# Performance work log

Measured on AMD Instinct MI355X. Metric: run time of the kernel, lower is better.

## Reference

```python
import jax, jax.numpy as jnp
import numpy as np

N0, N1, N2 = 120000, 40000, 10000   # sampled node counts per hop
E0, E1 = 600000, 150000             # edges per block (fanout ~15)
DIN, DH, NC = 128, 256, 47


def _glorot(k, fan_in, fan_out):
    s = (2.0 / (fan_in + fan_out)) ** 0.5
    return jax.random.normal(k, (fan_in, fan_out), jnp.float32) * s


def setup_inputs() -> dict:
    key = jax.random.key(0)
    ks = jax.random.split(key, 20)
    x0 = jax.random.normal(ks[0], (N0, DIN), jnp.float32)
    src0 = jax.random.randint(ks[1], (E0,), 0, N0)
    dst0 = jax.random.randint(ks[2], (E0,), 0, N1)
    src1 = jax.random.randint(ks[3], (E1,), 0, N1)
    dst1 = jax.random.randint(ks[4], (E1,), 0, N2)
    srcb0 = jax.random.randint(ks[5], (E0,), 0, N0)
    dstb0 = jax.random.randint(ks[6], (E0,), 0, N1)
    srcb1 = jax.random.randint(ks[7], (E1,), 0, N1)
    dstb1 = jax.random.randint(ks[8], (E1,), 0, N2)
    # id_old_value_new: must satisfy idx[:n] < n for every truncation length n,
    # i.e. idx[k] in [0, k+1)
    rng = np.random.default_rng(0)
    idx = jnp.asarray((rng.random(N0) * (np.arange(N0) + 1)).astype(np.int64))
    mix_ratio = jnp.float32(0.5)
    Wl0 = _glorot(ks[9], DIN, DH); Wr0 = _glorot(ks[10], DIN, DH)
    b0 = jnp.zeros((DH,), jnp.float32)
    Wl1 = _glorot(ks[11], DH, DH); Wr1 = _glorot(ks[12], DH, DH)
    b1 = jnp.zeros((DH,), jnp.float32)
    Wlin = _glorot(ks[13], DH, NC)
    blin = jnp.zeros((NC,), jnp.float32)
    return dict(x0=x0, src0=src0, dst0=dst0, src1=src1, dst1=dst1,
                srcb0=srcb0, dstb0=dstb0, srcb1=srcb1, dstb1=dstb1,
                idx=idx, mix_ratio=mix_ratio,
                Wl0=Wl0, Wr0=Wr0, b0=b0, Wl1=Wl1, Wr1=Wr1, b1=b1,
                Wlin=Wlin, blin=blin)


def _sage(x_all, root_x, src, dst, n_root, Wl, Wr, b):
    # PyG-style SAGEConv, mean aggregation: lin_l(mean_j x_j) + lin_r(root)
    msgs = x_all[src]                                        # [E, D] gather
    s = jax.ops.segment_sum(msgs, dst, num_segments=n_root)  # [n_root, D]
    cnt = jax.ops.segment_sum(jnp.ones_like(dst, dtype=x_all.dtype), dst,
                              num_segments=n_root)
    mean = s / jnp.maximum(cnt, 1.0)[:, None]
    return mean @ Wl + root_x @ Wr + b


def reference(x0, src0, dst0, src1, dst1, srcb0, dstb0, srcb1, dstb1,
              idx, mix_ratio, Wl0, Wr0, b0, Wl1, Wr1, b1, Wlin, blin):
    blocks = [(src0, dst0, N1), (src1, dst1, N2)]
    blocks_b = [(srcb0, dstb0, N1), (srcb1, dstb1, N2)]
    params = [(Wl0, Wr0, b0), (Wl1, Wr1, b1)]
    m = mix_ratio

    # first branch (dropout omitted: inference mode)
    aggr_xs = [x0]
    for i in range(2):
        src, dst, n_root = blocks[i]
        Wl, Wr, b = params[i]
        root_x = aggr_xs[-1][:n_root]
        x = jax.nn.relu(_sage(aggr_xs[-1], root_x, src, dst, n_root, Wl, Wr, b))
        aggr_xs.append(x)

    # permuted branch via id_old_value_new gather
    aggr_xs_b = [x[idx[: x.shape[0]]] for x in aggr_xs]

    x_mix = aggr_xs[0] * m + aggr_xs_b[0] * (1.0 - m)
    for i in range(2):
        src, dst, n_root = blocks[i]
        srcb, dstb, n_root_b = blocks_b[i]
        Wl, Wr, b = params[i]
        x_new = jax.nn.relu(_sage(aggr_xs[i], x_mix[:n_root], src, dst,
                                  n_root, Wl, Wr, b))
        x_new_b = jax.nn.relu(_sage(aggr_xs_b[i], x_mix[:n_root_b], srcb, dstb,
                                    n_root_b, Wl, Wr, b))
        x_mix = x_new * m + x_new_b * (1.0 - m)

    logits = x_mix @ Wlin + blin
    return jax.nn.log_softmax(logits, axis=-1)
```

## Files before the change

### kernel.cpp

```cpp
#include <hip/hip_runtime.h>
#include <math.h>

#define N1C 40000
#define N2C 10000
#define DIN 128
#define DH  256
#define NC  47

#define TOTCNT (2 * N1C + 2 * N2C)
#define CAP 64
#define CURSTR 16

typedef __attribute__((ext_vector_type(8))) short v8s;
typedef __attribute__((ext_vector_type(4))) float v4f;
typedef __attribute__((ext_vector_type(2))) float v2f;

#if __has_builtin(__builtin_amdgcn_cvt_pk_f32_fp8)
#define HW_FP8 1
#endif

__device__ __forceinline__ unsigned short f2bf(float f) {
    unsigned int u = __float_as_uint(f);
    u += 0x7FFF + ((u >> 16) & 1);
    return (unsigned short)(u >> 16);
}

__device__ __forceinline__ unsigned char f2e4m3(float f) {
    unsigned int u = __float_as_uint(f);
    unsigned char s = (unsigned char)((u >> 24) & 0x80);
    float a = __uint_as_float(u & 0x7FFFFFFF);
    if (a > 448.0f) a = 448.0f;
    if (a < 0.015625f) {
        int k = (int)rintf(a * 512.0f);
        return s | (unsigned char)k;
    }
    unsigned int bits = __float_as_uint(a);
    int et = (int)(bits >> 23) - 127 + 7;
    unsigned int m32 = bits & 0x7FFFFF;
    unsigned int m3 = m32 >> 20;
    unsigned int rest = m32 & 0xFFFFF;
    if (rest > 0x80000 || (rest == 0x80000 && (m3 & 1))) m3++;
    if (m3 == 8) { m3 = 0; et++; }
    if (et > 15 || (et == 15 && m3 == 7)) return s | 0x7E;
    return s | (unsigned char)((et << 3) | m3);
}

__device__ __forceinline__ unsigned int pack4_e4m3(float f0, float f1,
                                                   float f2, float f3) {
#if __has_builtin(__builtin_amdgcn_cvt_pk_fp8_f32)
    int q = __builtin_amdgcn_cvt_pk_fp8_f32(f0, f1, 0, false);
    q = __builtin_amdgcn_cvt_pk_fp8_f32(f2, f3, q, true);
    return (unsigned int)q;
#else
    return (unsigned int)f2e4m3(f0) | ((unsigned int)f2e4m3(f1) << 8) |
           ((unsigned int)f2e4m3(f2) << 16) | ((unsigned int)f2e4m3(f3) << 24);
#endif
}

__device__ __forceinline__ void dec4(unsigned int u, float& f0, float& f1,
                                     float& f2, float& f3) {
#ifdef HW_FP8
    v2f lo = __builtin_amdgcn_cvt_pk_f32_fp8((int)u, false);
    v2f hi = __builtin_amdgcn_cvt_pk_f32_fp8((int)u, true);
    f0 = lo[0]; f1 = lo[1]; f2 = hi[0]; f3 = hi[1];
#else
    auto d1 = [](unsigned int b) -> float {
        int e = (b >> 3) & 15, mm = b & 7;
        float d = (e == 0) ? (float)mm * (1.0f / 512.0f)
                           : (1.0f + (float)mm * 0.125f) * exp2f((float)(e - 7));
        return (b & 0x80) ? -d : d;
    };
    f0 = d1(u & 0xFF); f1 = d1((u >> 8) & 0xFF);
    f2 = d1((u >> 16) & 0xFF); f3 = d1(u >> 24);
#endif
}

__device__ __forceinline__ void acc16(uint4 q, float* a) {
    float f0, f1, f2, f3;
    dec4(q.x, f0, f1, f2, f3); a[0] += f0; a[1] += f1; a[2] += f2; a[3] += f3;
    dec4(q.y, f0, f1, f2, f3); a[4] += f0; a[5] += f1; a[6] += f2; a[7] += f3;
    dec4(q.z, f0, f1, f2, f3); a[8] += f0; a[9] += f1; a[10] += f2; a[11] += f3;
    dec4(q.w, f0, f1, f2, f3); a[12] += f0; a[13] += f1; a[14] += f2; a[15] += f3;
}

__global__ __launch_bounds__(256) void front_fused(
        const int* __restrict__ src0, const int* __restrict__ dst0,
        const int* __restrict__ srcb0, const int* __restrict__ dstb0,
        const int* __restrict__ src1, const int* __restrict__ dst1,
        const int* __restrict__ srcb1, const int* __restrict__ dstb1,
        const int* __restrict__ perm, int* __restrict__ cur,
        int* __restrict__ bucket, int E0, int E1, int nbMain,
        const float* __restrict__ x0, unsigned char* __restrict__ x0f,
        int n8,
        const float* __restrict__ Wl0, const float* __restrict__ Wr0,
        const float* __restrict__ Wl1, const float* __restrict__ Wr1,
        unsigned short* __restrict__ Wt0l, unsigned short* __restrict__ Wt0r,
        unsigned short* __restrict__ Wt1l, unsigned short* __restrict__ Wt1r) {
    int b = blockIdx.x, t = threadIdx.x;
    if (b < nbMain) {
        int gid = b * 256 + t;
        int tot = 2 * E0 + 2 * E1;
        bool doEdge = gid < tot;
        int s = 0, bin = 0, pos = CAP;
        if (doEdge) {
            if (gid < E0) {
                s = src0[gid];                bin = dst0[gid];
            } else if (gid < 2 * E0) {
                int le = gid - E0;
                s = perm[srcb0[le]];          bin = N1C + dstb0[le];
            } else if (gid < 2 * E0 + E1) {
                int le = gid - 2 * E0;
                s = src1[le];                 bin = 2 * N1C + dst1[le];
            } else {
                int le = gid - 2 * E0 - E1;
                s = perm[srcb1[le]];          bin = 2 * N1C + N2C + dstb1[le];
            }
            pos = atomicAdd(&cur[(size_t)bin * CURSTR], 1);
        }
        if (gid < n8) {
            const float4* p = (const float4*)(x0 + (size_t)gid * 8);
            float4 a = p[0], c = p[1];
            uint2 q;
            q.x = pack4_e4m3(a.x, a.y, a.z, a.w);
            q.y = pack4_e4m3(c.x, c.y, c.z, c.w);
            *(uint2*)(x0f + (size_t)gid * 8) = q;
        }
        if (doEdge && pos < CAP) bucket[(size_t)bin * CAP + pos] = s;
    } else {
        int id = (b - nbMain) * 256 + t;
        const int S0 = DIN * DH;
        const int S1 = DH * DH;
        const float* W; unsigned short* Wt; int K, loc;
        if (id < S0)                   { W = Wl0; Wt = Wt0l; K = DIN; loc = id; }
        else if (id < 2 * S0)          { W = Wr0; Wt = Wt0r; K = DIN; loc = id - S0; }
        else if (id < 2 * S0 + S1)     { W = Wl1; Wt = Wt1l; K = DH;  loc = id - 2 * S0; }
        else if (id < 2 * S0 + 2 * S1) { W = Wr1; Wt = Wt1r; K = DH;  loc = id - 2 * S0 - S1; }
        else return;
        int n = loc / K, k = loc - n * K;
        Wt[(size_t)n * K + k] = f2bf(W[(size_t)k * DH + n]);
    }
}

__global__ __launch_bounds__(256) void gather_mean_128f(
        const unsigned char* __restrict__ xf, const int* __restrict__ bucket,
        const int* __restrict__ cur, unsigned short* __restrict__ mean0,
        unsigned short* __restrict__ meanb0) {
    const int half = N1C / 32;
    int b = blockIdx.x;
    int binbase; unsigned short* outp; int rb;
    if (b < half) { binbase = 0;   outp = mean0;  rb = b; }
    else          { binbase = N1C; outp = meanb0; rb = b - half; }
    int wv = threadIdx.x >> 6, lane = threadIdx.x & 63;
    int row = rb * 32 + wv * 8 + (lane >> 3);
    int c16 = (lane & 7) * 16;
    int bin = binbase + row;
    int cnt = min(cur[(size_t)bin * CURSTR], CAP);
    const int* cs = bucket + (size_t)bin * CAP;
    float a[16];
#pragma unroll
    for (int j = 0; j < 16; j++) a[j] = 0.0f;
    int i = 0;
    for (; i + 3 < cnt; i += 4) {
        int s0 = cs[i], s1 = cs[i + 1], s2 = cs[i + 2], s3 = cs[i + 3];
        uint4 q0 = *(const uint4*)&xf[(size_t)s0 * DIN + c16];
        uint4 q1 = *(const uint4*)&xf[(size_t)s1 * DIN + c16];
        uint4 q2 = *(const uint4*)&xf[(size_t)s2 * DIN + c16];
        uint4 q3 = *(const uint4*)&xf[(size_t)s3 * DIN + c16];
        acc16(q0, a); acc16(q1, a); acc16(q2, a); acc16(q3, a);
    }
    for (; i < cnt; i++) {
        uint4 q = *(const uint4*)&xf[(size_t)cs[i] * DIN + c16];
        acc16(q, a);
    }
    float inv = 1.0f / (float)max(cnt, 1);
    uint4 o0, o1;
    o0.x = (unsigned int)f2bf(a[0] * inv)  | ((unsigned int)f2bf(a[1] * inv) << 16);
    o0.y = (unsigned int)f2bf(a[2] * inv)  | ((unsigned int)f2bf(a[3] * inv) << 16);
    o0.z = (unsigned int)f2bf(a[4] * inv)  | ((unsigned int)f2bf(a[5] * inv) << 16);
    o0.w = (unsigned int)f2bf(a[6] * inv)  | ((unsigned int)f2bf(a[7] * inv) << 16);
    o1.x = (unsigned int)f2bf(a[8] * inv)  | ((unsigned int)f2bf(a[9] * inv) << 16);
    o1.y = (unsigned int)f2bf(a[10] * inv) | ((unsigned int)f2bf(a[11] * inv) << 16);
    o1.z = (unsigned int)f2bf(a[12] * inv) | ((unsigned int)f2bf(a[13] * inv) << 16);
    o1.w = (unsigned int)f2bf(a[14] * inv) | ((unsigned int)f2bf(a[15] * inv) << 16);
    unsigned short* op = &outp[(size_t)row * DIN + c16];
    *(uint4*)op = o0;
    *(uint4*)(op + 8) = o1;
}

__global__ __launch_bounds__(256) void gather_mean_256f(
        const unsigned char* __restrict__ xf, const int* __restrict__ bucket,
        const int* __restrict__ cur, unsigned short* __restrict__ mean1,
        unsigned short* __restrict__ meanb1) {
    const int half = N2C / 16;
    int b = blockIdx.x;
    int binbase; unsigned short* outp; int rb;
    if (b < half) { binbase = 2 * N1C;       outp = mean1;  rb = b; }
    else          { binbase = 2 * N1C + N2C; outp = meanb1; rb = b - half; }
    int wv = threadIdx.x >> 6, lane = threadIdx.x & 63;
    int row = rb * 16 + wv * 4 + (lane >> 4);
    int c16 = (lane & 15) * 16;
    int bin = binbase + row;
    int cnt = min(cur[(size_t)bin * CURSTR], CAP);
    const int* cs = bucket + (size_t)bin * CAP;
    float a[16];
#pragma unroll
    for (int j = 0; j < 16; j++) a[j] = 0.0f;
    int i = 0;
    for (; i + 3 < cnt; i += 4) {
        int s0 = cs[i], s1 = cs[i + 1], s2 = cs[i + 2], s3 = cs[i + 3];
        uint4 q0 = *(const uint4*)&xf[(size_t)s0 * DH + c16];
        uint4 q1 = *(const uint4*)&xf[(size_t)s1 * DH + c16];
        uint4 q2 = *(const uint4*)&xf[(size_t)s2 * DH + c16];
        uint4 q3 = *(const uint4*)&xf[(size_t)s3 * DH + c16];
        acc16(q0, a); acc16(q1, a); acc16(q2, a); acc16(q3, a);
    }
    for (; i < cnt; i++) {
        uint4 q = *(const uint4*)&xf[(size_t)cs[i] * DH + c16];
        acc16(q, a);
    }
    float inv = 1.0f / (float)max(cnt, 1);
    uint4 o0, o1;
    o0.x = (unsigned int)f2bf(a[0] * inv)  | ((unsigned int)f2bf(a[1] * inv) << 16);
    o0.y = (unsigned int)f2bf(a[2] * inv)  | ((unsigned int)f2bf(a[3] * inv) << 16);
    o0.z = (unsigned int)f2bf(a[4] * inv)  | ((unsigned int)f2bf(a[5] * inv) << 16);
    o0.w = (unsigned int)f2bf(a[6] * inv)  | ((unsigned int)f2bf(a[7] * inv) << 16);
    o1.x = (unsigned int)f2bf(a[8] * inv)  | ((unsigned int)f2bf(a[9] * inv) << 16);
    o1.y = (unsigned int)f2bf(a[10] * inv) | ((unsigned int)f2bf(a[11] * inv) << 16);
    o1.z = (unsigned int)f2bf(a[12] * inv) | ((unsigned int)f2bf(a[13] * inv) << 16);
    o1.w = (unsigned int)f2bf(a[14] * inv) | ((unsigned int)f2bf(a[15] * inv) << 16);
    unsigned short* op = &outp[(size_t)row * DH + c16];
    *(uint4*)op = o0;
    *(uint4*)(op + 8) = o1;
}

#define KP0 136
#define H0T 5
__global__ __launch_bounds__(256, 2) void hop0_mfma(
        const float* __restrict__ x0, const int* __restrict__ idx,
        const unsigned short* __restrict__ mean0, const unsigned short* __restrict__ meanb0,
        const unsigned short* __restrict__ Wtl, const unsigned short* __restrict__ Wtr,
        const float* __restrict__ b, const float* __restrict__ mixp,
        unsigned char* __restrict__ x1f, unsigned short* __restrict__ xm1) {
    __shared__ unsigned short Alds[4][16][KP0];
    int t = threadIdx.x;
    int wv = t >> 6, lane = t & 63;
    int mrow = lane & 15, quad = lane >> 4;
    float m = *mixp;

    v8s wl[4][4], wr[4][4];
    float bb[4];
#pragma unroll
    for (int ct = 0; ct < 4; ct++) {
        int n = wv * 64 + mrow * 4 + ct;
        bb[ct] = b[n];
#pragma unroll
        for (int ks = 0; ks < 4; ks++) {
            int k0 = ks * 32 + quad * 8;
            wl[ct][ks] = *(const v8s*)&Wtl[(size_t)n * DIN + k0];
            wr[ct][ks] = *(const v8s*)&Wtr[(size_t)n * DIN + k0];
        }
    }

    for (int tile = 0; tile < H0T; tile++) {
        int row0 = (blockIdx.x * H0T + tile) * 16;
        {
            int r = t >> 4, k0 = (t & 15) * 8;
            int rg = row0 + r;
            *(v8s*)&Alds[0][r][k0] = *(const v8s*)&mean0[(size_t)rg * DIN + k0];
            *(v8s*)&Alds[1][r][k0] = *(const v8s*)&meanb0[(size_t)rg * DIN + k0];
            const float4* xr4 = (const float4*)&x0[(size_t)rg * DIN + k0];
            float4 A0 = xr4[0], A1 = xr4[1];
            int ib = idx[rg];
            const float4* xb4 = (const float4*)&x0[(size_t)ib * DIN + k0];
            float4 B0 = xb4[0], B1 = xb4[1];
            float fa[8] = {A0.x, A0.y, A0.z, A0.w, A1.x, A1.y, A1.z, A1.w};
            float fb[8] = {B0.x, B0.y, B0.z, B0.w, B1.x, B1.y, B1.z, B1.w};
            v8s vr, vm;
#pragma unroll
            for (int j = 0; j < 8; j++) {
                vr[j] = (short)f2bf(fa[j]);
                vm[j] = (short)f2bf(m * fa[j] + (1.0f - m) * fb[j]);
            }
            *(v8s*)&Alds[2][r][k0] = vr;
            *(v8s*)&Alds[3][r][k0] = vm;
        }
        __syncthreads();
        v4f accA[4], accB[4], accC[4], accD[4];
#pragma unroll
        for (int ct = 0; ct < 4; ct++) {
            accA[ct] = (v4f){0.f, 0.f, 0.f, 0.f}; accB[ct] = (v4f){0.f, 0.f, 0.f, 0.f};
            accC[ct] = (v4f){0.f, 0.f, 0.f, 0.f}; accD[ct] = (v4f){0.f, 0.f, 0.f, 0.f};
        }
#pragma unroll
        for (int ks = 0; ks < 4; ks++) {
            int k0 = ks * 32 + quad * 8;
            v8s aM = *(v8s*)&Alds[0][mrow][k0];
            v8s aB = *(v8s*)&Alds[1][mrow][k0];
            v8s aR = *(v8s*)&Alds[2][mrow][k0];
            v8s aX = *(v8s*)&Alds[3][mrow][k0];
#pragma unroll
            for (int ct = 0; ct < 4; ct++) {
                accA[ct] = __builtin_amdgcn_mfma_f32_16x16x32_bf16(aM, wl[ct][ks], accA[ct], 0, 0, 0);
                accB[ct] = __builtin_amdgcn_mfma_f32_16x16x32_bf16(aB, wl[ct][ks], accB[ct], 0, 0, 0);
                accC[ct] = __builtin_amdgcn_mfma_f32_16x16x32_bf16(aR, wr[ct][ks], accC[ct], 0, 0, 0);
                accD[ct] = __builtin_amdgcn_mfma_f32_16x16x32_bf16(aX, wr[ct][ks], accD[ct], 0, 0, 0);
            }
        }
        int colb = wv * 64 + mrow * 4;
#pragma unroll
        for (int r = 0; r < 4; r++) {
            int row = row0 + quad * 4 + r;
            float xv[4];
            unsigned short sh[4];
#pragma unroll
            for (int ct = 0; ct < 4; ct++) {
                float pA = accA[ct][r], pB = accB[ct][r], pC = accC[ct][r], pD = accD[ct][r];
                xv[ct]    = fmaxf(pA + pC + bb[ct], 0.0f);
                float xn  = fmaxf(pA + pD + bb[ct], 0.0f);
                float xnb = fmaxf(pB + pD + bb[ct], 0.0f);
                sh[ct] = f2bf(m * xn + (1.0f - m) * xnb);
            }
            unsigned int xpack = pack4_e4m3(xv[0], xv[1], xv[2], xv[3]);
            unsigned int s01 = (unsigned int)sh[0] | ((unsigned int)sh[1] << 16);
            unsigned int s23 = (unsigned int)sh[2] | ((unsigned int)sh[3] << 16);
            *(unsigned int*)&x1f[(size_t)row * DH + colb] = xpack;
            uint2 xm = {s01, s23};
            *(uint2*)&xm1[(size_t)row * DH + colb] = xm;
        }
        __syncthreads();
    }
}

#define KP1 264
#define H1T 2
__global__ __launch_bounds__(256, 2) void hop1_mfma(
        const unsigned short* __restrict__ mean1, const unsigned short* __restrict__ meanb1,
        const unsigned short* __restrict__ xm1,
        const unsigned short* __restrict__ Wtl, const unsigned short* __restrict__ Wtr,
        const float* __restrict__ b, const float* __restrict__ mixp,
        float* __restrict__ xm2) {
    __shared__ unsigned short Alds[3][16][KP1];
    int t = threadIdx.x;
    int wv = t >> 6, lane = t & 63;
    int mrow = lane & 15, quad = lane >> 4;
    float m = *mixp;

    v8s wlc[4][4], wrc[4][4];
    float bb[4];
#pragma unroll
    for (int ct = 0; ct < 4; ct++) {
        int n = wv * 64 + mrow * 4 + ct;
        bb[ct] = b[n];
#pragma unroll
        for (int ks = 0; ks < 4; ks++) {
            int k0 = ks * 32 + quad * 8;
            wlc[ct][ks] = *(const v8s*)&Wtl[(size_t)n * DH + k0];
            wrc[ct][ks] = *(const v8s*)&Wtr[(size_t)n * DH + k0];
        }
    }

    for (int tt = 0; tt < H1T; tt++) {
        int tIdx = blockIdx.x * H1T + tt;
        if (tIdx >= N2C / 16) break;
        int row0 = tIdx * 16;
        {
            int r = t >> 4, k0 = (t & 15) * 16;
            int rg = row0 + r;
            *(v8s*)&Alds[0][r][k0]     = *(const v8s*)&mean1[(size_t)rg * DH + k0];
            *(v8s*)&Alds[0][r][k0 + 8] = *(const v8s*)&mean1[(size_t)rg * DH + k0 + 8];
            *(v8s*)&Alds[1][r][k0]     = *(const v8s*)&meanb1[(size_t)rg * DH + k0];
            *(v8s*)&Alds[1][r][k0 + 8] = *(const v8s*)&meanb1[(size_t)rg * DH + k0 + 8];
            *(v8s*)&Alds[2][r][k0]     = *(const v8s*)&xm1[(size_t)rg * DH + k0];
            *(v8s*)&Alds[2][r][k0 + 8] = *(const v8s*)&xm1[(size_t)rg * DH + k0 + 8];
        }
        __syncthreads();
        v4f accA[4], accB[4], accC[4];
#pragma unroll
        for (int ct = 0; ct < 4; ct++) {
            accA[ct] = (v4f){0.f, 0.f, 0.f, 0.f};
            accB[ct] = (v4f){0.f, 0.f, 0.f, 0.f};
            accC[ct] = (v4f){0.f, 0.f, 0.f, 0.f};
        }
#pragma unroll
        for (int ks = 0; ks < 8; ks++) {
            int k0 = ks * 32 + quad * 8;
            v8s aM = *(v8s*)&Alds[0][mrow][k0];
            v8s aB = *(v8s*)&Alds[1][mrow][k0];
            v8s aR = *(v8s*)&Alds[2][mrow][k0];
#pragma unroll
            for (int ct = 0; ct < 4; ct++) {
                v8s bl, br;
                if (ks < 4) { bl = wlc[ct][ks]; br = wrc[ct][ks]; }
                else {
                    int n = wv * 64 + mrow * 4 + ct;
                    bl = *(const v8s*)&Wtl[(size_t)n * DH + k0];
                    br = *(const v8s*)&Wtr[(size_t)n * DH + k0];
                }
                accA[ct] = __builtin_amdgcn_mfma_f32_16x16x32_bf16(aM, bl, accA[ct], 0, 0, 0);
                accB[ct] = __builtin_amdgcn_mfma_f32_16x16x32_bf16(aB, bl, accB[ct], 0, 0, 0);
                accC[ct] = __builtin_amdgcn_mfma_f32_16x16x32_bf16(aR, br, accC[ct], 0, 0, 0);
            }
        }
        int colb = wv * 64 + mrow * 4;
#pragma unroll
        for (int r = 0; r < 4; r++) {
            int row = row0 + quad * 4 + r;
            float4 o;
            float v0 = fmaxf(accA[0][r] + accC[0][r] + bb[0], 0.0f);
            float w0 = fmaxf(accB[0][r] + accC[0][r] + bb[0], 0.0f);
            float v1 = fmaxf(accA[1][r] + accC[1][r] + bb[1], 0.0f);
            float w1 = fmaxf(accB[1][r] + accC[1][r] + bb[1], 0.0f);
            float v2 = fmaxf(accA[2][r] + accC[2][r] + bb[2], 0.0f);
            float w2 = fmaxf(accB[2][r] + accC[2][r] + bb[2], 0.0f);
            float v3 = fmaxf(accA[3][r] + accC[3][r] + bb[3], 0.0f);
            float w3 = fmaxf(accB[3][r] + accC[3][r] + bb[3], 0.0f);
            o.x = m * v0 + (1.0f - m) * w0;
            o.y = m * v1 + (1.0f - m) * w1;
            o.z = m * v2 + (1.0f - m) * w2;
            o.w = m * v3 + (1.0f - m) * w3;
            *(float4*)&xm2[(size_t)row * DH + colb] = o;
        }
        __syncthreads();
    }
}

__global__ __launch_bounds__(256) void logits_lsm(
        const float* __restrict__ xmix2, const float* __restrict__ Wlin,
        const float* __restrict__ blin, float* __restrict__ out, int nrows) {
    int w = threadIdx.x >> 6;
    int row = blockIdx.x * 4 + w;
    int t = threadIdx.x & 63;
    __shared__ float xs[4][DH];
    if (row < nrows)
        for (int i = t; i < DH; i += 64) xs[w][i] = xmix2[(size_t)row * DH + i];
    __syncthreads();
    if (row >= nrows) return;
    float acc = 0.0f;
    if (t < NC) {
        acc = blin[t];
        for (int k = 0; k < DH; k++) acc += xs[w][k] * Wlin[k * NC + t];
    }
    float v = (t < NC) ? acc : -INFINITY;
    float mx = v;
    for (int off = 32; off; off >>= 1) mx = fmaxf(mx, __shfl_xor(mx, off, 64));
    float ex = (t < NC) ? expf(acc - mx) : 0.0f;
    float sum = ex;
    for (int off = 32; off; off >>= 1) sum += __shfl_xor(sum, off, 64);
    if (t < NC) out[(size_t)row * NC + t] = acc - mx - logf(sum);
}

extern "C" void kernel_launch(void* const* d_in, const int* in_sizes, int n_in,
                              void* d_out, int out_size, void* d_ws, size_t ws_size,
                              hipStream_t stream) {
    const float* x0    = (const float*)d_in[0];
    const int*   src0  = (const int*)d_in[1];
    const int*   dst0  = (const int*)d_in[2];
    const int*   src1  = (const int*)d_in[3];
    const int*   dst1  = (const int*)d_in[4];
    const int*   srcb0 = (const int*)d_in[5];
    const int*   dstb0 = (const int*)d_in[6];
    const int*   srcb1 = (const int*)d_in[7];
    const int*   dstb1 = (const int*)d_in[8];
    const int*   idx   = (const int*)d_in[9];
    const float* mixp  = (const float*)d_in[10];
    const float* Wl0   = (const float*)d_in[11];
    const float* Wr0   = (const float*)d_in[12];
    const float* b0    = (const float*)d_in[13];
    const float* Wl1   = (const float*)d_in[14];
    const float* Wr1   = (const float*)d_in[15];
    const float* b1    = (const float*)d_in[16];
    const float* Wlin  = (const float*)d_in[17];
    const float* blin  = (const float*)d_in[18];
    float* out = (float*)d_out;

    const int E0 = in_sizes[1];
    const int E1 = in_sizes[3];
    const long x0elems = (long)in_sizes[0];

    int* wsi    = (int*)d_ws;
    int* cur    = wsi;
    int* bucket = cur + (size_t)TOTCNT * CURSTR;
    unsigned short* wsh = (unsigned short*)(bucket + (size_t)TOTCNT * CAP);
    unsigned short* mean0  = wsh;
    unsigned short* meanb0 = mean0  + (size_t)N1C * DIN;
    unsigned short* mean1  = meanb0 + (size_t)N1C * DIN;
    unsigned short* meanb1 = mean1  + (size_t)N2C * DH;
    unsigned short* xm1h   = meanb1 + (size_t)N2C * DH;
    unsigned short* Wt0l   = xm1h   + (size_t)N1C * DH;
    unsigned short* Wt0r   = Wt0l + DIN * DH;
    unsigned short* Wt1l   = Wt0r + DIN * DH;
    unsigned short* Wt1r   = Wt1l + DH * DH;
    float* xm2 = (float*)(Wt1r + DH * DH);
    unsigned char* x0f = (unsigned char*)(xm2 + (size_t)N2C * DH);
    unsigned char* x1f = x0f + (size_t)x0elems;

    hipMemsetAsync(cur, 0, sizeof(int) * (size_t)TOTCNT * CURSTR, stream);

    int etot = 2 * E0 + 2 * E1;
    int n8 = (int)(x0elems / 8);
    int nbEdges = (etot + 255) / 256;
    int nbConv = (n8 + 255) / 256;
    int nbMain = nbEdges > nbConv ? nbEdges : nbConv;
    int nbW = (2 * DIN * DH + 2 * DH * DH + 255) / 256;
    front_fused<<<nbMain + nbW, 256, 0, stream>>>(
        src0, dst0, srcb0, dstb0, src1, dst1, srcb1, dstb1, idx, cur, bucket,
        E0, E1, nbMain, x0, x0f, n8,
        Wl0, Wr0, Wl1, Wr1, Wt0l, Wt0r, Wt1l, Wt1r);

    gather_mean_128f<<<2 * (N1C / 32), 256, 0, stream>>>(x0f, bucket, cur, mean0, meanb0);

    hop0_mfma<<<N1C / (16 * H0T), 256, 0, stream>>>(x0, idx, mean0, meanb0, Wt0l, Wt0r,
                                                    b0, mixp, x1f, xm1h);

    gather_mean_256f<<<2 * (N2C / 16), 256, 0, stream>>>(x1f, bucket, cur, mean1, meanb1);

    hop1_mfma<<<(N2C / 16 + H1T - 1) / H1T, 256, 0, stream>>>(mean1, meanb1, xm1h,
                                                              Wt1l, Wt1r, b1, mixp, xm2);

    logits_lsm<<<(N2C + 3) / 4, 256, 0, stream>>>(xm2, Wlin, blin, out, N2C);
}
```

Baseline: 320.3 us.

## Replicate edge bucket counters across block-indexed replicas to cut atomic contention

Edge bucketing now spreads each destination's counter and bucket over eight replicas chosen by block index, instead of one padded counter per bin with a 16-int stride. The gather kernels merge the replicas into a shared-memory index list before accumulating. This targets same-address atomic contention and shrinks the memset, which was 16x larger than needed. It also stores only the first N2C rows of the bf16 mixed hop-0 output, since only those are used later, and shrinks that buffer. The risk is that the per-replica capacity of 16 can overflow for skewed destinations where the old cap of 64 would not, and the gathers gain a serial merge step.

```diff
diff --git a/kernel.cpp b/kernel.cpp
--- a/kernel.cpp
+++ b/kernel.cpp
@@ -9,7 +9,8 @@
 
 #define TOTCNT (2 * N1C + 2 * N2C)
 #define CAP 64
-#define CURSTR 16
+#define NREP 8
+#define CAPR 16
 
 typedef __attribute__((ext_vector_type(8))) short v8s;
 typedef __attribute__((ext_vector_type(4))) float v4f;
@@ -99,9 +100,10 @@
     int b = blockIdx.x, t = threadIdx.x;
     if (b < nbMain) {
         int gid = b * 256 + t;
+        int rep = b & (NREP - 1);
         int tot = 2 * E0 + 2 * E1;
         bool doEdge = gid < tot;
-        int s = 0, bin = 0, pos = CAP;
+        int s = 0, bin = 0, pos = CAPR;
         if (doEdge) {
             if (gid < E0) {
                 s = src0[gid];                bin = dst0[gid];
@@ -115,7 +117,7 @@
                 int le = gid - 2 * E0 - E1;
                 s = perm[srcb1[le]];          bin = 2 * N1C + N2C + dstb1[le];
             }
-            pos = atomicAdd(&cur[(size_t)bin * CURSTR], 1);
+            pos = atomicAdd(&cur[(size_t)rep * TOTCNT + bin], 1);
         }
         if (gid < n8) {
             const float4* p = (const float4*)(x0 + (size_t)gid * 8);
@@ -125,7 +127,8 @@
             q.y = pack4_e4m3(c.x, c.y, c.z, c.w);
             *(uint2*)(x0f + (size_t)gid * 8) = q;
         }
-        if (doEdge && pos < CAP) bucket[(size_t)bin * CAP + pos] = s;
+        if (doEdge && pos < CAPR)
+            bucket[((size_t)rep * TOTCNT + bin) * CAPR + pos] = s;
     } else {
         int id = (b - nbMain) * 256 + t;
         const int S0 = DIN * DH;
@@ -150,12 +153,27 @@
     int binbase; unsigned short* outp; int rb;
     if (b < half) { binbase = 0;   outp = mean0;  rb = b; }
     else          { binbase = N1C; outp = meanb0; rb = b - half; }
-    int wv = threadIdx.x >> 6, lane = threadIdx.x & 63;
-    int row = rb * 32 + wv * 8 + (lane >> 3);
-    int c16 = (lane & 7) * 16;
-    int bin = binbase + row;
-    int cnt = min(cur[(size_t)bin * CURSTR], CAP);
-    const int* cs = bucket + (size_t)bin * CAP;
+    int t = threadIdx.x;
+    __shared__ int midx[32][NREP * CAPR];
+    __shared__ int mcnt[32];
+    {
+        int rloc = t >> 3, rep = t & 7;
+        int bin = binbase + rb * 32 + rloc;
+        int off = 0, cr = 0;
+        for (int j = 0; j <= rep; j++) {
+            int c = min(cur[(size_t)j * TOTCNT + bin], CAPR);
+            if (j < rep) off += c; else cr = c;
+        }
+        const int* bp = &bucket[((size_t)rep * TOTCNT + bin) * CAPR];
+        for (int k = 0; k < cr; k++) midx[rloc][off + k] = bp[k];
+        if (rep == 7) mcnt[rloc] = off + cr;
+    }
+    __syncthreads();
+    int rloc = t >> 3;
+    int row = rb * 32 + rloc;
+    int c16 = (t & 7) * 16;
+    int cnt = mcnt[rloc];
+    const int* cs = &midx[rloc][0];
     float a[16];
 #pragma unroll
     for (int j = 0; j < 16; j++) a[j] = 0.0f;
@@ -196,12 +214,30 @@
     int binbase; unsigned short* outp; int rb;
     if (b < half) { binbase = 2 * N1C;       outp = mean1;  rb = b; }
     else          { binbase = 2 * N1C + N2C; outp = meanb1; rb = b - half; }
-    int wv = threadIdx.x >> 6, lane = threadIdx.x & 63;
-    int row = rb * 16 + wv * 4 + (lane >> 4);
-    int c16 = (lane & 15) * 16;
-    int bin = binbase + row;
-    int cnt = min(cur[(size_t)bin * CURSTR], CAP);
-    const int* cs = bucket + (size_t)bin * CAP;
+    int t = threadIdx.x;
+    __shared__ int midx[16][NREP * CAPR];
+    __shared__ int mcnt[16];
+    {
+        int rloc = t >> 4, sub = t & 15;
+        if (sub < 8) {
+            int rep = sub;
+            int bin = binbase + rb * 16 + rloc;
+            int off = 0, cr = 0;
+            for (int j = 0; j <= rep; j++) {
+                int c = min(cur[(size_t)j * TOTCNT + bin], CAPR);
+                if (j < rep) off += c; else cr = c;
+            }
+            const int* bp = &bucket[((size_t)rep * TOTCNT + bin) * CAPR];
+            for (int k = 0; k < cr; k++) midx[rloc][off + k] = bp[k];
+            if (rep == 7) mcnt[rloc] = off + cr;
+        }
+    }
+    __syncthreads();
+    int rloc = t >> 4;
+    int row = rb * 16 + rloc;
+    int c16 = (t & 15) * 16;
+    int cnt = mcnt[rloc];
+    const int* cs = &midx[rloc][0];
     float a[16];
 #pragma unroll
     for (int j = 0; j < 16; j++) a[j] = 0.0f;
@@ -321,11 +357,13 @@
                 sh[ct] = f2bf(m * xn + (1.0f - m) * xnb);
             }
             unsigned int xpack = pack4_e4m3(xv[0], xv[1], xv[2], xv[3]);
-            unsigned int s01 = (unsigned int)sh[0] | ((unsigned int)sh[1] << 16);
-            unsigned int s23 = (unsigned int)sh[2] | ((unsigned int)sh[3] << 16);
             *(unsigned int*)&x1f[(size_t)row * DH + colb] = xpack;
-            uint2 xm = {s01, s23};
-            *(uint2*)&xm1[(size_t)row * DH + colb] = xm;
+            if (row < N2C) {
+                unsigned int s01 = (unsigned int)sh[0] | ((unsigned int)sh[1] << 16);
+                unsigned int s23 = (unsigned int)sh[2] | ((unsigned int)sh[3] << 16);
+                uint2 xm = {s01, s23};
+                *(uint2*)&xm1[(size_t)row * DH + colb] = xm;
+            }
         }
         __syncthreads();
     }
@@ -479,14 +517,14 @@
 
     int* wsi    = (int*)d_ws;
     int* cur    = wsi;
-    int* bucket = cur + (size_t)TOTCNT * CURSTR;
-    unsigned short* wsh = (unsigned short*)(bucket + (size_t)TOTCNT * CAP);
+    int* bucket = cur + (size_t)NREP * TOTCNT;
+    unsigned short* wsh = (unsigned short*)(bucket + (size_t)NREP * TOTCNT * CAPR);
     unsigned short* mean0  = wsh;
     unsigned short* meanb0 = mean0  + (size_t)N1C * DIN;
     unsigned short* mean1  = meanb0 + (size_t)N1C * DIN;
     unsigned short* meanb1 = mean1  + (size_t)N2C * DH;
     unsigned short* xm1h   = meanb1 + (size_t)N2C * DH;
-    unsigned short* Wt0l   = xm1h   + (size_t)N1C * DH;
+    unsigned short* Wt0l   = xm1h   + (size_t)N2C * DH;
     unsigned short* Wt0r   = Wt0l + DIN * DH;
     unsigned short* Wt1l   = Wt0r + DIN * DH;
     unsigned short* Wt1r   = Wt1l + DH * DH;
@@ -494,7 +532,7 @@
     unsigned char* x0f = (unsigned char*)(xm2 + (size_t)N2C * DH);
     unsigned char* x1f = x0f + (size_t)x0elems;
 
-    hipMemsetAsync(cur, 0, sizeof(int) * (size_t)TOTCNT * CURSTR, stream);
+    hipMemsetAsync(cur, 0, sizeof(int) * (size_t)NREP * TOTCNT, stream);
 
     int etot = 2 * E0 + 2 * E1;
     int n8 = (int)(x0elems / 8);
```

Result: no change. 324.8 us (+1.4%).

## Slice bucket fill by destination range and pack counters densely

Applied to the files above, without the earlier changes.

The edge bucketing is reorganised so each group of blocks reads a 2048-edge chunk and only inserts edges whose destination bin falls in its slice of eight, which gives the atomics on the now densely packed counters locality. The padded counter stride is removed, shrinking the memset and the counter footprint. The xm1 mix buffer is also stored only for rows below N2C, since only those are read later, which cuts write traffic. In exchange, every destination index is read eight times and the per-edge control flow grows.

```diff
diff --git a/kernel.cpp b/kernel.cpp
--- a/kernel.cpp
+++ b/kernel.cpp
@@ -9,7 +9,8 @@
 
 #define TOTCNT (2 * N1C + 2 * N2C)
 #define CAP 64
-#define CURSTR 16
+#define NSLICE 8
+#define SLICEW (TOTCNT / NSLICE)
 
 typedef __attribute__((ext_vector_type(8))) short v8s;
 typedef __attribute__((ext_vector_type(4))) float v4f;
@@ -99,24 +100,6 @@
     int b = blockIdx.x, t = threadIdx.x;
     if (b < nbMain) {
         int gid = b * 256 + t;
-        int tot = 2 * E0 + 2 * E1;
-        bool doEdge = gid < tot;
-        int s = 0, bin = 0, pos = CAP;
-        if (doEdge) {
-            if (gid < E0) {
-                s = src0[gid];                bin = dst0[gid];
-            } else if (gid < 2 * E0) {
-                int le = gid - E0;
-                s = perm[srcb0[le]];          bin = N1C + dstb0[le];
-            } else if (gid < 2 * E0 + E1) {
-                int le = gid - 2 * E0;
-                s = src1[le];                 bin = 2 * N1C + dst1[le];
-            } else {
-                int le = gid - 2 * E0 - E1;
-                s = perm[srcb1[le]];          bin = 2 * N1C + N2C + dstb1[le];
-            }
-            pos = atomicAdd(&cur[(size_t)bin * CURSTR], 1);
-        }
         if (gid < n8) {
             const float4* p = (const float4*)(x0 + (size_t)gid * 8);
             float4 a = p[0], c = p[1];
@@ -125,7 +108,31 @@
             q.y = pack4_e4m3(c.x, c.y, c.z, c.w);
             *(uint2*)(x0f + (size_t)gid * 8) = q;
         }
-        if (doEdge && pos < CAP) bucket[(size_t)bin * CAP + pos] = s;
+        int tot = 2 * E0 + 2 * E1;
+        int binLo = (b & (NSLICE - 1)) * SLICEW;
+        int wbase = (b >> 3) * 2048;
+        if (wbase < tot) {
+#pragma unroll
+            for (int j = 0; j < 8; j++) {
+                int e = wbase + j * 256 + t;
+                if (e < tot) {
+                    int bin;
+                    if (e < E0)               bin = dst0[e];
+                    else if (e < 2 * E0)      bin = N1C + dstb0[e - E0];
+                    else if (e < 2 * E0 + E1) bin = 2 * N1C + dst1[e - 2 * E0];
+                    else                      bin = 2 * N1C + N2C + dstb1[e - 2 * E0 - E1];
+                    if ((unsigned)(bin - binLo) < (unsigned)SLICEW) {
+                        int s;
+                        if (e < E0)               s = src0[e];
+                        else if (e < 2 * E0)      s = perm[srcb0[e - E0]];
+                        else if (e < 2 * E0 + E1) s = src1[e - 2 * E0];
+                        else                      s = perm[srcb1[e - 2 * E0 - E1]];
+                        int pos = atomicAdd(&cur[bin], 1);
+                        if (pos < CAP) bucket[(size_t)bin * CAP + pos] = s;
+                    }
+                }
+            }
+        }
     } else {
         int id = (b - nbMain) * 256 + t;
         const int S0 = DIN * DH;
@@ -154,7 +161,7 @@
     int row = rb * 32 + wv * 8 + (lane >> 3);
     int c16 = (lane & 7) * 16;
     int bin = binbase + row;
-    int cnt = min(cur[(size_t)bin * CURSTR], CAP);
+    int cnt = min(cur[bin], CAP);
     const int* cs = bucket + (size_t)bin * CAP;
     float a[16];
 #pragma unroll
@@ -200,7 +207,7 @@
     int row = rb * 16 + wv * 4 + (lane >> 4);
     int c16 = (lane & 15) * 16;
     int bin = binbase + row;
-    int cnt = min(cur[(size_t)bin * CURSTR], CAP);
+    int cnt = min(cur[bin], CAP);
     const int* cs = bucket + (size_t)bin * CAP;
     float a[16];
 #pragma unroll
@@ -321,11 +328,13 @@
                 sh[ct] = f2bf(m * xn + (1.0f - m) * xnb);
             }
             unsigned int xpack = pack4_e4m3(xv[0], xv[1], xv[2], xv[3]);
-            unsigned int s01 = (unsigned int)sh[0] | ((unsigned int)sh[1] << 16);
-            unsigned int s23 = (unsigned int)sh[2] | ((unsigned int)sh[3] << 16);
             *(unsigned int*)&x1f[(size_t)row * DH + colb] = xpack;
-            uint2 xm = {s01, s23};
-            *(uint2*)&xm1[(size_t)row * DH + colb] = xm;
+            if (row < N2C) {
+                unsigned int s01 = (unsigned int)sh[0] | ((unsigned int)sh[1] << 16);
+                unsigned int s23 = (unsigned int)sh[2] | ((unsigned int)sh[3] << 16);
+                uint2 xm = {s01, s23};
+                *(uint2*)&xm1[(size_t)row * DH + colb] = xm;
+            }
         }
         __syncthreads();
     }
@@ -479,14 +488,14 @@
 
     int* wsi    = (int*)d_ws;
     int* cur    = wsi;
-    int* bucket = cur + (size_t)TOTCNT * CURSTR;
+    int* bucket = cur + TOTCNT;
     unsigned short* wsh = (unsigned short*)(bucket + (size_t)TOTCNT * CAP);
     unsigned short* mean0  = wsh;
     unsigned short* meanb0 = mean0  + (size_t)N1C * DIN;
     unsigned short* mean1  = meanb0 + (size_t)N1C * DIN;
     unsigned short* meanb1 = mean1  + (size_t)N2C * DH;
     unsigned short* xm1h   = meanb1 + (size_t)N2C * DH;
-    unsigned short* Wt0l   = xm1h   + (size_t)N1C * DH;
+    unsigned short* Wt0l   = xm1h   + (size_t)N2C * DH;
     unsigned short* Wt0r   = Wt0l + DIN * DH;
     unsigned short* Wt1l   = Wt0r + DIN * DH;
     unsigned short* Wt1r   = Wt1l + DH * DH;
@@ -494,13 +503,13 @@
     unsigned char* x0f = (unsigned char*)(xm2 + (size_t)N2C * DH);
     unsigned char* x1f = x0f + (size_t)x0elems;
 
-    hipMemsetAsync(cur, 0, sizeof(int) * (size_t)TOTCNT * CURSTR, stream);
+    hipMemsetAsync(cur, 0, sizeof(int) * (size_t)TOTCNT, stream);
 
     int etot = 2 * E0 + 2 * E1;
     int n8 = (int)(x0elems / 8);
-    int nbEdges = (etot + 255) / 256;
+    int nbFill = ((etot + 2047) / 2048) * NSLICE;
     int nbConv = (n8 + 255) / 256;
-    int nbMain = nbEdges > nbConv ? nbEdges : nbConv;
+    int nbMain = nbFill > nbConv ? nbFill : nbConv;
     int nbW = (2 * DIN * DH + 2 * DH * DH + 255) / 256;
     front_fused<<<nbMain + nbW, 256, 0, stream>>>(
         src0, dst0, srcb0, dstb0, src1, dst1, srcb1, dstb1, idx, cur, bucket,
```

New measurement: 322.1 us. About the same (+0.5%).
